# Kernel optimization log

Hardware: AMD Instinct MI355X
Metric: run time of the kernel (lower is better)

The kernel has to match this reference:

```python
import jax, jax.numpy as jnp
import numpy as np

T, B, D, H = 256, 64, 1024, 1024  # seq_len, batch, input_dim, hidden_dim (= n_qubits)


def setup_inputs() -> dict:
    key = jax.random.key(0)
    ks = jax.random.split(key, 9)
    scale = 1.0 / np.sqrt(D + H)
    inp = {
        "inputs": jax.random.normal(ks[0], (T, B, D), dtype=jnp.float32),
        # nn.Linear weights (out=H wires, in=D+H) and biases, per gate
        "Wf": jax.random.normal(ks[1], (H, D + H), dtype=jnp.float32) * scale,
        "bf": jnp.zeros((H,), dtype=jnp.float32),
        "gbf": jnp.zeros((H,), dtype=jnp.float32),  # QLinearGate bias (init zeros)
        "Wi": jax.random.normal(ks[2], (H, D + H), dtype=jnp.float32) * scale,
        "bi": jnp.zeros((H,), dtype=jnp.float32),
        "gbi": jnp.zeros((H,), dtype=jnp.float32),
        "Wu": jax.random.normal(ks[3], (H, D + H), dtype=jnp.float32) * scale,
        "bu": jnp.zeros((H,), dtype=jnp.float32),
        "gbu": jnp.zeros((H,), dtype=jnp.float32),
        "Wo": jax.random.normal(ks[4], (H, D + H), dtype=jnp.float32) * scale,
        "bo": jnp.zeros((H,), dtype=jnp.float32),
        "gbo": jnp.zeros((H,), dtype=jnp.float32),
    }
    return inp


def reference(inputs, Wf, bf, gbf, Wi, bi, gbi, Wu, bu, gbu, Wo, bo, gbo):
    # QLinearGate: RY(theta)|0> -> <Z> = cos(theta); matmul with identity; add bias.
    def qgate(z, gb):
        return jnp.cos(z) + gb

    def step(carry, x):
        hx, cx = carry
        comb = jnp.concatenate([x, hx], axis=1)  # (B, D+H)
        f = jax.nn.sigmoid(qgate(comb @ Wf.T + bf, gbf))
        i = jax.nn.sigmoid(qgate(comb @ Wi.T + bi, gbi))
        g = jnp.tanh(qgate(comb @ Wu.T + bu, gbu))
        o = jax.nn.sigmoid(qgate(comb @ Wo.T + bo, gbo))
        cx = f * cx + i * g
        hx = o * jnp.tanh(cx)
        return (hx, cx), hx

    Bdim = inputs.shape[1]
    init = (jnp.zeros((Bdim, H), inputs.dtype), jnp.zeros((Bdim, H), inputs.dtype))
    (hx, cx), outputs = jax.lax.scan(step, init, inputs)
    return outputs, (hx, cx)
```

## Files before the change

kernel.cpp:

```cpp
#include <hip/hip_runtime.h>
#include <cmath>
#include <cstring>

constexpr int TT = 256;
constexpr int BB = 64;
constexpr int DD = 1024;
constexpr int HH = 1024;
constexpr int KK = DD + HH;
constexpr int NBLK = 256;
constexpr int NTHR = 512;
constexpr int CK = 64;
constexpr int NCHF = KK / CK;
constexpr int HPB = 4;

constexpr int WS_UINTS = TT * 8 * 16 + TT * 16;

__device__ __forceinline__ float sigm(float v) { return 1.0f / (1.0f + expf(-v)); }

__device__ __forceinline__ float qsum4(float x) {
  int v = __builtin_amdgcn_mov_dpp(__float_as_int(x), 0xB1, 0xF, 0xF, true);
  x += __int_as_float(v);
  v = __builtin_amdgcn_mov_dpp(__float_as_int(x), 0x4E, 0xF, 0xF, true);
  x += __int_as_float(v);
  return x;
}

__device__ __forceinline__ void gridbar(unsigned* ws, int t, int tid, int bid) {
  __syncthreads();
  if (tid == 0) {
    asm volatile("s_waitcnt vmcnt(0)" ::: "memory");
    unsigned* grp  = ws + (size_t)(t * 8 + (bid >> 5)) * 16;
    unsigned* done = ws + 32768 + (size_t)t * 16;
    unsigned old = __hip_atomic_fetch_add(grp, 1u, __ATOMIC_RELAXED, __HIP_MEMORY_SCOPE_AGENT);
    if (old == 31u)
      __hip_atomic_fetch_add(done, 1u, __ATOMIC_RELAXED, __HIP_MEMORY_SCOPE_AGENT);
    while (__hip_atomic_load(done, __ATOMIC_RELAXED, __HIP_MEMORY_SCOPE_AGENT) < 8u)
      __builtin_amdgcn_s_sleep(1);
    asm volatile("" ::: "memory");
  }
  __syncthreads();
}

__global__ void zero_ws(unsigned* p, int n) {
  int i = blockIdx.x * blockDim.x + threadIdx.x;
  if (i < n) p[i] = 0u;
}

__global__ __launch_bounds__(NTHR, 2)
void qlstm_fused3(const float* __restrict__ x,
                  const float* __restrict__ Wf, const float* __restrict__ bf, const float* __restrict__ gbf,
                  const float* __restrict__ Wi, const float* __restrict__ bi, const float* __restrict__ gbi,
                  const float* __restrict__ Wu, const float* __restrict__ bu, const float* __restrict__ gbu,
                  const float* __restrict__ Wo, const float* __restrict__ bo, const float* __restrict__ gbo,
                  float* __restrict__ out, unsigned* __restrict__ ws)
{
  __shared__ float lds[40960];
  float* const Wl   = lds;
  float* const cbA  = lds + 32768;
  float* const cbB  = lds + 36864;
  float* const zbuf = lds + 32768;

  const int tid  = threadIdx.x;
  const int lane = tid & 63;
  const int rg   = tid >> 6;
  const int cgp  = lane >> 4;
  const int kp   = lane & 15;
  const int srow = tid >> 3;
  const int sseg = tid & 7;
  const int bid  = blockIdx.x;
  const int h0   = bid * HPB;

  {
    const float* Wg[4] = {Wf, Wi, Wu, Wo};
    #pragma unroll
    for (int j = 0; j < 16; ++j) {
      const float4 w = *(const float4*)(Wg[j >> 2] + (size_t)(h0 + (j & 3)) * KK + tid * 4);
      *(float4*)&Wl[j * KK + tid * 4] = w;
    }
  }

  const int urow = tid >> 2;
  const int uhl  = tid & 3;
  const int hcell = h0 + uhl;
  float bfv = 0, gbfv = 0, biv = 0, gbiv = 0, buv = 0, gbuv = 0, bov = 0, gbov = 0;
  if (tid < 256) {
    bfv = bf[hcell]; gbfv = gbf[hcell];
    biv = bi[hcell]; gbiv = gbi[hcell];
    buv = bu[hcell]; gbuv = gbu[hcell];
    bov = bo[hcell]; gbov = gbo[hcell];
  }
  float cx = 0.0f, hxl = 0.0f;

  auto ld8 = [](const float* p) -> float2 {
    unsigned long long u = __hip_atomic_load((const unsigned long long*)(const void*)p,
                                             __ATOMIC_RELAXED, __HIP_MEMORY_SCOPE_AGENT);
    float2 r; __builtin_memcpy(&r, &u, 8); return r;
  };

  for (int t = 0; t < TT; ++t) {
    const int nch = (t == 0) ? (DD / CK) : NCHF;

    float acc[8][4];
    #pragma unroll
    for (int i = 0; i < 8; ++i)
      #pragma unroll
      for (int j = 0; j < 4; ++j) acc[i][j] = 0.0f;

    auto loadChunk = [&](int kc, float4& va, float4& vb) {
      const int k0 = kc * CK;
      if (k0 < DD) {
        const float* base = x + (size_t)t * BB * DD + (size_t)srow * DD + k0;
        va = *(const float4*)(base + sseg * 4);
        vb = *(const float4*)(base + 32 + sseg * 4);
      } else {
        const float* base = out + (size_t)(t - 1) * BB * HH + (size_t)srow * HH + (k0 - DD);
        const float2 a0 = ld8(base + sseg * 4);
        const float2 a1 = ld8(base + sseg * 4 + 2);
        const float2 b0 = ld8(base + 32 + sseg * 4);
        const float2 b1 = ld8(base + 32 + sseg * 4 + 2);
        va = {a0.x, a0.y, a1.x, a1.y};
        vb = {b0.x, b0.y, b1.x, b1.y};
      }
    };
    auto storeChunk = [&](float* cb, const float4 va, const float4 vb) {
      *(float4*)&cb[srow * CK + sseg * 4]      = va;
      *(float4*)&cb[srow * CK + 32 + sseg * 4] = vb;
    };

    float4 va, vb;
    loadChunk(0, va, vb);
    storeChunk(cbA, va, vb);
    loadChunk(1, va, vb);

    for (int kc = 0; kc < nch; ++kc) {
      float* const cbW = (kc & 1) ? cbA : cbB;
      float* const cbR = (kc & 1) ? cbB : cbA;
      if (kc + 1 < nch) storeChunk(cbW, va, vb);
      if (kc + 2 < nch) loadChunk(kc + 2, va, vb);

      const int cko = kc * CK;
      float4 cfr[8];
      #pragma unroll
      for (int i = 0; i < 8; ++i)
        cfr[i] = *(const float4*)&cbR[(rg * 8 + i) * CK + kp * 4];
      #pragma unroll
      for (int j = 0; j < 4; ++j) {
        const float4 w = *(const float4*)&Wl[(cgp * 4 + j) * KK + cko + kp * 4];
        #pragma unroll
        for (int i = 0; i < 8; ++i) {
          acc[i][j] = fmaf(cfr[i].x, w.x, acc[i][j]);
          acc[i][j] = fmaf(cfr[i].y, w.y, acc[i][j]);
          acc[i][j] = fmaf(cfr[i].z, w.z, acc[i][j]);
          acc[i][j] = fmaf(cfr[i].w, w.w, acc[i][j]);
        }
      }
    }

    #pragma unroll
    for (int i = 0; i < 8; ++i)
      #pragma unroll
      for (int j = 0; j < 4; ++j) acc[i][j] = qsum4(acc[i][j]);

    __syncthreads();
    if ((lane & 3) == 0) {
      const int kpg = (lane >> 2) & 3;
      #pragma unroll
      for (int i = 0; i < 8; ++i) {
        const float4 v = {acc[i][0], acc[i][1], acc[i][2], acc[i][3]};
        *(float4*)&zbuf[(size_t)((kpg * 64) + rg * 8 + i) * 16 + cgp * 4] = v;
      }
    }
    __syncthreads();

    if (tid < 256) {
      float zf = bfv, zi = biv, zu = buv, zo = bov;
      #pragma unroll
      for (int p = 0; p < 4; ++p) {
        const float* zr = &zbuf[(size_t)(p * 64 + urow) * 16];
        zf += zr[0 + uhl];
        zi += zr[4 + uhl];
        zu += zr[8 + uhl];
        zo += zr[12 + uhl];
      }
      const float fg = sigm(cosf(zf) + gbfv);
      const float ig = sigm(cosf(zi) + gbiv);
      const float gg = tanhf(cosf(zu) + gbuv);
      const float og = sigm(cosf(zo) + gbov);
      cx = fg * cx + ig * gg;
      const float hx = og * tanhf(cx);
      __hip_atomic_store(&out[(size_t)t * BB * HH + (size_t)urow * HH + hcell], hx,
                         __ATOMIC_RELAXED, __HIP_MEMORY_SCOPE_AGENT);
      hxl = hx;
    }

    gridbar(ws, t, tid, bid);
  }

  if (tid < 256) {
    float* hxout = out + (size_t)TT * BB * HH;
    float* cxout = hxout + (size_t)BB * HH;
    hxout[(size_t)urow * HH + hcell] = hxl;
    cxout[(size_t)urow * HH + hcell] = cx;
  }
}

extern "C" void kernel_launch(void* const* d_in, const int* in_sizes, int n_in,
                              void* d_out, int out_size, void* d_ws, size_t ws_size,
                              hipStream_t stream) {
  const float* x   = (const float*)d_in[0];
  const float* Wf  = (const float*)d_in[1];
  const float* bf_ = (const float*)d_in[2];
  const float* gbf = (const float*)d_in[3];
  const float* Wi  = (const float*)d_in[4];
  const float* bi_ = (const float*)d_in[5];
  const float* gbi = (const float*)d_in[6];
  const float* Wu  = (const float*)d_in[7];
  const float* bu_ = (const float*)d_in[8];
  const float* gbu = (const float*)d_in[9];
  const float* Wo  = (const float*)d_in[10];
  const float* bo_ = (const float*)d_in[11];
  const float* gbo = (const float*)d_in[12];
  float* out = (float*)d_out;
  unsigned* wsp = (unsigned*)d_ws;

  zero_ws<<<(WS_UINTS + 255) / 256, 256, 0, stream>>>(wsp, WS_UINTS);

  void* args[] = {&x, &Wf, &bf_, &gbf, &Wi, &bi_, &gbi, &Wu, &bu_, &gbu,
                  &Wo, &bo_, &gbo, &out, &wsp};
  hipLaunchCooperativeKernel((void*)qlstm_fused3, dim3(NBLK), dim3(NTHR),
                             args, 0, stream);
}
```

Baseline: 5.489 ms.

## Precompute input projections per 8-step segment outside the recurrent barrier chain

```diff
diff --git a/kernel.cpp b/kernel.cpp
--- a/kernel.cpp
+++ b/kernel.cpp
@@ -6,14 +6,16 @@
 constexpr int BB = 64;
 constexpr int DD = 1024;
 constexpr int HH = 1024;
-constexpr int KK = DD + HH;
+constexpr int KK = 2048;
 constexpr int NBLK = 256;
 constexpr int NTHR = 512;
 constexpr int CK = 64;
-constexpr int NCHF = KK / CK;
+constexpr int NCH = 16;
+constexpr int SEG = 8;
+constexpr int NSEG = TT / SEG;
 constexpr int HPB = 4;
 
-constexpr int WS_UINTS = TT * 8 * 16 + TT * 16;
+constexpr int FLAG_UINTS = TT * 8 * 16 + TT * 16;
 
 __device__ __forceinline__ float sigm(float v) { return 1.0f / (1.0f + expf(-v)); }
 
@@ -47,7 +49,7 @@
 }
 
 __global__ __launch_bounds__(NTHR, 2)
-void qlstm_fused3(const float* __restrict__ x,
+void qlstm_fused4(const float* __restrict__ x,
                   const float* __restrict__ Wf, const float* __restrict__ bf, const float* __restrict__ gbf,
                   const float* __restrict__ Wi, const float* __restrict__ bi, const float* __restrict__ gbi,
                   const float* __restrict__ Wu, const float* __restrict__ bu, const float* __restrict__ gbu,
@@ -70,6 +72,8 @@
   const int bid  = blockIdx.x;
   const int h0   = bid * HPB;
 
+  float* const wsz = (float*)ws + FLAG_UINTS;
+
   {
     const float* Wg[4] = {Wf, Wi, Wu, Wo};
     #pragma unroll
@@ -96,104 +100,175 @@
                                              __ATOMIC_RELAXED, __HIP_MEMORY_SCOPE_AGENT);
     float2 r; __builtin_memcpy(&r, &u, 8); return r;
   };
-
-  for (int t = 0; t < TT; ++t) {
-    const int nch = (t == 0) ? (DD / CK) : NCHF;
-
-    float acc[8][4];
-    #pragma unroll
-    for (int i = 0; i < 8; ++i)
+  auto storeChunk = [&](float* cb, const float4 va, const float4 vb) {
+    *(float4*)&cb[srow * CK + sseg * 4]      = va;
+    *(float4*)&cb[srow * CK + 32 + sseg * 4] = vb;
+  };
+
+  __syncthreads();
+
+  for (int seg = 0; seg < NSEG; ++seg) {
+    for (int s = 0; s < SEG; ++s) {
+      const int t = seg * SEG + s;
+      float acc[8][4];
       #pragma unroll
-      for (int j = 0; j < 4; ++j) acc[i][j] = 0.0f;
-
-    auto loadChunk = [&](int kc, float4& va, float4& vb) {
-      const int k0 = kc * CK;
-      if (k0 < DD) {
-        const float* base = x + (size_t)t * BB * DD + (size_t)srow * DD + k0;
+      for (int i = 0; i < 8; ++i)
+        #pragma unroll
+        for (int j = 0; j < 4; ++j) acc[i][j] = 0.0f;
+
+      auto loadChunkX = [&](int kc, float4& va, float4& vb) {
+        const float* base = x + (size_t)t * BB * DD + (size_t)srow * DD + kc * CK;
         va = *(const float4*)(base + sseg * 4);
         vb = *(const float4*)(base + 32 + sseg * 4);
-      } else {
-        const float* base = out + (size_t)(t - 1) * BB * HH + (size_t)srow * HH + (k0 - DD);
-        const float2 a0 = ld8(base + sseg * 4);
-        const float2 a1 = ld8(base + sseg * 4 + 2);
-        const float2 b0 = ld8(base + 32 + sseg * 4);
-        const float2 b1 = ld8(base + 32 + sseg * 4 + 2);
-        va = {a0.x, a0.y, a1.x, a1.y};
-        vb = {b0.x, b0.y, b1.x, b1.y};
-      }
-    };
-    auto storeChunk = [&](float* cb, const float4 va, const float4 vb) {
-      *(float4*)&cb[srow * CK + sseg * 4]      = va;
-      *(float4*)&cb[srow * CK + 32 + sseg * 4] = vb;
-    };
-
-    float4 va, vb;
-    loadChunk(0, va, vb);
-    storeChunk(cbA, va, vb);
-    loadChunk(1, va, vb);
-
-    for (int kc = 0; kc < nch; ++kc) {
-      float* const cbW = (kc & 1) ? cbA : cbB;
-      float* const cbR = (kc & 1) ? cbB : cbA;
-      if (kc + 1 < nch) storeChunk(cbW, va, vb);
-      if (kc + 2 < nch) loadChunk(kc + 2, va, vb);
-
-      const int cko = kc * CK;
-      float4 cfr[8];
+      };
+      auto computeChunk = [&](const float* cbR, int kbase) {
+        float4 cfr[8];
+        #pragma unroll
+        for (int i = 0; i < 8; ++i)
+          cfr[i] = *(const float4*)&cbR[(rg * 8 + i) * CK + kp * 4];
+        #pragma unroll
+        for (int j = 0; j < 4; ++j) {
+          const float4 w = *(const float4*)&Wl[(cgp * 4 + j) * KK + kbase + kp * 4];
+          #pragma unroll
+          for (int i = 0; i < 8; ++i) {
+            acc[i][j] = fmaf(cfr[i].x, w.x, acc[i][j]);
+            acc[i][j] = fmaf(cfr[i].y, w.y, acc[i][j]);
+            acc[i][j] = fmaf(cfr[i].z, w.z, acc[i][j]);
+            acc[i][j] = fmaf(cfr[i].w, w.w, acc[i][j]);
+          }
+        }
+      };
+
+      float4 va, vb;
+      loadChunkX(0, va, vb);
+      storeChunk(cbA, va, vb);
+      loadChunkX(1, va, vb);
+      for (int kc = 0; kc < NCH; ++kc) {
+        float* const cbW = (kc & 1) ? cbA : cbB;
+        float* const cbR = (kc & 1) ? cbB : cbA;
+        if (kc + 1 < NCH) storeChunk(cbW, va, vb);
+        if (kc + 2 < NCH) loadChunkX(kc + 2, va, vb);
+        computeChunk(cbR, kc * CK);
+      }
+
       #pragma unroll
       for (int i = 0; i < 8; ++i)
-        cfr[i] = *(const float4*)&cbR[(rg * 8 + i) * CK + kp * 4];
+        #pragma unroll
+        for (int j = 0; j < 4; ++j) acc[i][j] = qsum4(acc[i][j]);
+      __syncthreads();
+      if ((lane & 3) == 0) {
+        const int kpg = (lane >> 2) & 3;
+        #pragma unroll
+        for (int i = 0; i < 8; ++i) {
+          const float4 v = {acc[i][0], acc[i][1], acc[i][2], acc[i][3]};
+          *(float4*)&zbuf[(size_t)((kpg * 64) + rg * 8 + i) * 16 + cgp * 4] = v;
+        }
+      }
+      __syncthreads();
+      if (tid < 256) {
+        float zf = 0, zi = 0, zu = 0, zo = 0;
+        #pragma unroll
+        for (int p = 0; p < 4; ++p) {
+          const float* zr = &zbuf[(size_t)(p * 64 + urow) * 16];
+          zf += zr[0 + uhl];
+          zi += zr[4 + uhl];
+          zu += zr[8 + uhl];
+          zo += zr[12 + uhl];
+        }
+        const float4 z4 = {zf, zi, zu, zo};
+        *(float4*)&wsz[((size_t)(bid * SEG + s) * 256 + tid) * 4] = z4;
+      }
+      __syncthreads();
+    }
+
+    for (int s = 0; s < SEG; ++s) {
+      const int t = seg * SEG + s;
+      float acc[8][4];
       #pragma unroll
-      for (int j = 0; j < 4; ++j) {
-        const float4 w = *(const float4*)&Wl[(cgp * 4 + j) * KK + cko + kp * 4];
+      for (int i = 0; i < 8; ++i)
+        #pragma unroll
+        for (int j = 0; j < 4; ++j) acc[i][j] = 0.0f;
+
+      if (t > 0) {
+        auto loadChunkH = [&](int kc, float4& va, float4& vb) {
+          const float* base = out + (size_t)(t - 1) * BB * HH + (size_t)srow * HH + kc * CK;
+          const float2 a0 = ld8(base + sseg * 4);
+          const float2 a1 = ld8(base + sseg * 4 + 2);
+          const float2 b0 = ld8(base + 32 + sseg * 4);
+          const float2 b1 = ld8(base + 32 + sseg * 4 + 2);
+          va = {a0.x, a0.y, a1.x, a1.y};
+          vb = {b0.x, b0.y, b1.x, b1.y};
+        };
+        auto computeChunk = [&](const float* cbR, int kbase) {
+          float4 cfr[8];
+          #pragma unroll
+          for (int i = 0; i < 8; ++i)
+            cfr[i] = *(const float4*)&cbR[(rg * 8 + i) * CK + kp * 4];
+          #pragma unroll
+          for (int j = 0; j < 4; ++j) {
+            const float4 w = *(const float4*)&Wl[(cgp * 4 + j) * KK + kbase + kp * 4];
+            #pragma unroll
+            for (int i = 0; i < 8; ++i) {
+              acc[i][j] = fmaf(cfr[i].x, w.x, acc[i][j]);
+              acc[i][j] = fmaf(cfr[i].y, w.y, acc[i][j]);
+              acc[i][j] = fmaf(cfr[i].z, w.z, acc[i][j]);
+              acc[i][j] = fmaf(cfr[i].w, w.w, acc[i][j]);
+            }
+          }
+        };
+
+        float4 va, vb;
+        loadChunkH(0, va, vb);
+        storeChunk(cbA, va, vb);
+        loadChunkH(1, va, vb);
+        for (int kc = 0; kc < NCH; ++kc) {
+          float* const cbW = (kc & 1) ? cbA : cbB;
+          float* const cbR = (kc & 1) ? cbB : cbA;
+          if (kc + 1 < NCH) storeChunk(cbW, va, vb);
+          if (kc + 2 < NCH) loadChunkH(kc + 2, va, vb);
+          computeChunk(cbR, DD + kc * CK);
+        }
+      }
+
+      #pragma unroll
+      for (int i = 0; i < 8; ++i)
+        #pragma unroll
+        for (int j = 0; j < 4; ++j) acc[i][j] = qsum4(acc[i][j]);
+      __syncthreads();
+      if ((lane & 3) == 0) {
+        const int kpg = (lane >> 2) & 3;
         #pragma unroll
         for (int i = 0; i < 8; ++i) {
-          acc[i][j] = fmaf(cfr[i].x, w.x, acc[i][j]);
-          acc[i][j] = fmaf(cfr[i].y, w.y, acc[i][j]);
-          acc[i][j] = fmaf(cfr[i].z, w.z, acc[i][j]);
-          acc[i][j] = fmaf(cfr[i].w, w.w, acc[i][j]);
-        }
-      }
+          const float4 v = {acc[i][0], acc[i][1], acc[i][2], acc[i][3]};
+          *(float4*)&zbuf[(size_t)((kpg * 64) + rg * 8 + i) * 16 + cgp * 4] = v;
+        }
+      }
+      __syncthreads();
+
+      if (tid < 256) {
+        const float4 z4 = *(const float4*)&wsz[((size_t)(bid * SEG + s) * 256 + tid) * 4];
+        float zf = bfv + z4.x, zi = biv + z4.y, zu = buv + z4.z, zo = bov + z4.w;
+        #pragma unroll
+        for (int p = 0; p < 4; ++p) {
+          const float* zr = &zbuf[(size_t)(p * 64 + urow) * 16];
+          zf += zr[0 + uhl];
+          zi += zr[4 + uhl];
+          zu += zr[8 + uhl];
+          zo += zr[12 + uhl];
+        }
+        const float fg = sigm(cosf(zf) + gbfv);
+        const float ig = sigm(cosf(zi) + gbiv);
+        const float gg = tanhf(cosf(zu) + gbuv);
+        const float og = sigm(cosf(zo) + gbov);
+        cx = fg * cx + ig * gg;
+        const float hx = og * tanhf(cx);
+        __hip_atomic_store(&out[(size_t)t * BB * HH + (size_t)urow * HH + hcell], hx,
+                           __ATOMIC_RELAXED, __HIP_MEMORY_SCOPE_AGENT);
+        hxl = hx;
+      }
+
+      gridbar(ws, t, tid, bid);
     }
-
-    #pragma unroll
-    for (int i = 0; i < 8; ++i)
-      #pragma unroll
-      for (int j = 0; j < 4; ++j) acc[i][j] = qsum4(acc[i][j]);
-
-    __syncthreads();
-    if ((lane & 3) == 0) {
-      const int kpg = (lane >> 2) & 3;
-      #pragma unroll
-      for (int i = 0; i < 8; ++i) {
-        const float4 v = {acc[i][0], acc[i][1], acc[i][2], acc[i][3]};
-        *(float4*)&zbuf[(size_t)((kpg * 64) + rg * 8 + i) * 16 + cgp * 4] = v;
-      }
-    }
-    __syncthreads();
-
-    if (tid < 256) {
-      float zf = bfv, zi = biv, zu = buv, zo = bov;
-      #pragma unroll
-      for (int p = 0; p < 4; ++p) {
-        const float* zr = &zbuf[(size_t)(p * 64 + urow) * 16];
-        zf += zr[0 + uhl];
-        zi += zr[4 + uhl];
-        zu += zr[8 + uhl];
-        zo += zr[12 + uhl];
-      }
-      const float fg = sigm(cosf(zf) + gbfv);
-      const float ig = sigm(cosf(zi) + gbiv);
-      const float gg = tanhf(cosf(zu) + gbuv);
-      const float og = sigm(cosf(zo) + gbov);
-      cx = fg * cx + ig * gg;
-      const float hx = og * tanhf(cx);
-      __hip_atomic_store(&out[(size_t)t * BB * HH + (size_t)urow * HH + hcell], hx,
-                         __ATOMIC_RELAXED, __HIP_MEMORY_SCOPE_AGENT);
-      hxl = hx;
-    }
-
-    gridbar(ws, t, tid, bid);
   }
 
   if (tid < 256) {
@@ -223,10 +298,10 @@
   float* out = (float*)d_out;
   unsigned* wsp = (unsigned*)d_ws;
 
-  zero_ws<<<(WS_UINTS + 255) / 256, 256, 0, stream>>>(wsp, WS_UINTS);
+  zero_ws<<<(FLAG_UINTS + 255) / 256, 256, 0, stream>>>(wsp, FLAG_UINTS);
 
   void* args[] = {&x, &Wf, &bf_, &gbf, &Wi, &bi_, &gbi, &Wu, &bu_, &gbu,
                   &Wo, &bo_, &gbo, &out, &wsp};
-  hipLaunchCooperativeKernel((void*)qlstm_fused3, dim3(NBLK), dim3(NTHR),
+  hipLaunchCooperativeKernel((void*)qlstm_fused4, dim3(NBLK), dim3(NTHR),
                              args, 0, stream);
 }
```

After: 5.687 ms. +3.6%, slower.
